# Optimization experiments

Hardware: AMD Instinct MI355X
Metric: run time of the kernel (lower is better)

Reference implementation:

```python
import jax, jax.numpy as jnp
import numpy as np

N_EMBD = 512
HEAD_SIZE = 64
T = 4096
B = 4


def setup_inputs() -> dict:
    key = jax.random.key(0)
    kx, kq, kk, kv = jax.random.split(key, 4)
    x = jax.random.normal(kx, (B, T, N_EMBD), dtype=jnp.float32)
    # torch nn.Linear(n_embd, head_size, bias=False): weight [head_size, n_embd];
    # stored here transposed as [n_embd, head_size] so projection is x @ W.
    s = 1.0 / np.sqrt(N_EMBD)
    Wq = jax.random.uniform(kq, (N_EMBD, HEAD_SIZE), jnp.float32, -s, s)
    Wk = jax.random.uniform(kk, (N_EMBD, HEAD_SIZE), jnp.float32, -s, s)
    Wv = jax.random.uniform(kv, (N_EMBD, HEAD_SIZE), jnp.float32, -s, s)
    return {"x": x, "Wq": Wq, "Wk": Wk, "Wv": Wv}


def reference(x, Wq, Wk, Wv):
    Bq, Tq, C = x.shape
    q = x @ Wq  # [B,T,H]
    k = x @ Wk  # [B,T,H]
    v = x @ Wv  # [B,T,H]
    # NOTE: original scales by C**-0.5 with C = n_embd (input dim), not head_size.
    wei = jnp.einsum('bqh,bkh->bqk', q, k) * (C ** -0.5)  # [B,T,T]
    causal = jnp.tril(jnp.ones((Tq, Tq), dtype=bool))
    wei = jnp.where(causal, wei, -jnp.inf)
    wei = jax.nn.softmax(wei, axis=-1)
    # dropout p=0.0 -> identity (eval-mode deterministic baseline)
    out = jnp.einsum('bqk,bkh->bqh', wei, v)  # [B,T,H]
    return out
```

## Files before the change

kernel.cpp:

```cpp
#include <hip/hip_runtime.h>
#include <hip/hip_bf16.h>
#include <math.h>

#define T_SEQ 4096
#define NBATCH 4
#define C_EMB 512
#define HEAD 64
#define CHUNK 8
#define EPB 288

typedef __attribute__((ext_vector_type(8))) short short8;
typedef __attribute__((ext_vector_type(4))) short short4v;
typedef __attribute__((ext_vector_type(4))) float f32x4;

#define C2 (0.044194173824159216f * 1.44269504088896340736f)

__device__ __forceinline__ unsigned short f2bf(float f) {
    union { float f; unsigned u; } v; v.f = f;
    unsigned u = v.u;
    u += 0x7FFF + ((u >> 16) & 1);
    return (unsigned short)(u >> 16);
}
__device__ __forceinline__ unsigned pk2bf(float a, float b) {
    __hip_bfloat162 h = __float22bfloat162_rn(make_float2(a, b));
    return *(unsigned*)&h;
}

__global__ __launch_bounds__(64) void wcvt_kernel(
    const float* __restrict__ Wq, const float* __restrict__ Wk,
    const float* __restrict__ Wv, unsigned short* __restrict__ wt)
{
    const int w = blockIdx.x >> 6;
    const int n = blockIdx.x & 63;
    const float* W = (w == 0) ? Wq : (w == 1) ? Wk : Wv;
    const int k0 = threadIdx.x * 8;
    unsigned short tmp[8];
#pragma unroll
    for (int i = 0; i < 8; ++i) tmp[i] = f2bf(W[(size_t)(k0 + i) * HEAD + n]);
    *(short8*)(wt + ((size_t)blockIdx.x) * C_EMB + k0) = *(short8*)tmp;
}

__device__ __forceinline__ void ld_stage(const float* xp, int s, float4* xr) {
#pragma unroll
    for (int j = 0; j < 4; ++j) {
        xr[2 * j]     = *(const float4*)(xp + (s * 4 + j) * 32);
        xr[2 * j + 1] = *(const float4*)(xp + (s * 4 + j) * 32 + 4);
    }
}

__device__ __forceinline__ void mm_stage(const float4* xr, int s, int l16, int quad,
                                         const unsigned short* __restrict__ wt,
                                         f32x4 acc[3][4]) {
#pragma unroll
    for (int j = 0; j < 4; ++j) {
        const int kc = s * 4 + j;
        float4 a = xr[2 * j], b = xr[2 * j + 1];
        int4 ai = make_int4((int)pk2bf(a.x, a.y), (int)pk2bf(a.z, a.w),
                            (int)pk2bf(b.x, b.y), (int)pk2bf(b.z, b.w));
        short8 af = *(short8*)&ai;
#pragma unroll
        for (int w = 0; w < 3; ++w)
#pragma unroll
            for (int n = 0; n < 4; ++n) {
                short8 bf = *(const short8*)(wt + ((size_t)(w * 64 + n * 16 + l16)) * C_EMB
                                                + kc * 32 + quad * 8);
                acc[w][n] = __builtin_amdgcn_mfma_f32_16x16x32_bf16(af, bf, acc[w][n], 0, 0, 0);
            }
    }
}

__global__ __launch_bounds__(256) void proj_kernel(
    const float* __restrict__ x,
    const unsigned short* __restrict__ wt,
    unsigned short* __restrict__ qout,
    unsigned short* __restrict__ kout,
    unsigned short* __restrict__ vt)
{
    __shared__ unsigned short Vsh[64][72];

    const int tid  = threadIdx.x;
    const int wave = tid >> 6;
    const int lane = tid & 63;
    const int l16  = lane & 15;
    const int quad = lane >> 4;
    const int row0 = blockIdx.x * 64;
    const int rowW = row0 + wave * 16 + l16;

    f32x4 acc[3][4];
#pragma unroll
    for (int w = 0; w < 3; ++w)
#pragma unroll
        for (int n = 0; n < 4; ++n) acc[w][n] = (f32x4){0.f, 0.f, 0.f, 0.f};

    const float* xp = x + (size_t)rowW * C_EMB + quad * 8;
    float4 xr[2][8];
    ld_stage(xp, 0, xr[0]);
#pragma unroll
    for (int s = 0; s < 4; ++s) {
        if (s < 3) ld_stage(xp, s + 1, xr[(s + 1) & 1]);
        mm_stage(xr[s & 1], s, l16, quad, wt, acc);
    }

#pragma unroll
    for (int n = 0; n < 4; ++n)
#pragma unroll
        for (int r = 0; r < 4; ++r) {
            int row = row0 + wave * 16 + quad * 4 + r;
            qout[(size_t)row * HEAD + n * 16 + l16] = f2bf(acc[0][n][r] * C2);
            kout[(size_t)row * HEAD + n * 16 + l16] = f2bf(acc[1][n][r]);
        }

#pragma unroll
    for (int n = 0; n < 4; ++n)
#pragma unroll
        for (int r = 0; r < 4; ++r)
            Vsh[n * 16 + l16][wave * 16 + quad * 4 + r] = f2bf(acc[2][n][r]);
    __syncthreads();
    {
        int h  = tid >> 2;
        int tc = (tid & 3) * 16;
        int b  = row0 >> 12;
        int t0 = row0 & (T_SEQ - 1);
        unsigned short* dst = vt + ((size_t)(b * HEAD + h)) * T_SEQ + t0 + tc;
        *(short8*)dst       = *(const short8*)&Vsh[h][tc];
        *(short8*)(dst + 8) = *(const short8*)&Vsh[h][tc + 8];
    }
}

__device__ __forceinline__ void stage_v(unsigned short (*Vbuf)[72], int sr, int phiA,
                                        short8 v0, short8 v1) {
    *(short4v*)&Vbuf[sr][phiA]      = __builtin_shufflevector(v0, v0, 0, 1, 2, 3);
    *(short4v*)&Vbuf[sr][phiA + 8]  = __builtin_shufflevector(v0, v0, 4, 5, 6, 7);
    *(short4v*)&Vbuf[sr][phiA + 16] = __builtin_shufflevector(v1, v1, 0, 1, 2, 3);
    *(short4v*)&Vbuf[sr][phiA + 24] = __builtin_shufflevector(v1, v1, 4, 5, 6, 7);
}

__global__ __launch_bounds__(256) void attn1_kernel(
    const unsigned short* __restrict__ qb,
    const unsigned short* __restrict__ kb,
    const unsigned short* __restrict__ vt,
    float* __restrict__ po,
    float* __restrict__ pl)
{
    __shared__ unsigned short Ks[2][64][72];
    __shared__ unsigned short Vs[2][64][72];

    const int tid  = threadIdx.x;
    const int wave = tid >> 6;
    const int lane = tid & 63;
    const int l16  = lane & 15;
    const int quad = lane >> 4;

    const int b = blockIdx.x / EPB;
    const int e = blockIdx.x % EPB;
    int g = 0;
#pragma unroll
    for (int gg = 1; gg < 8; ++gg) if (e >= 4 * gg * (gg + 1)) g = gg;
    const int rem = e - 4 * g * (g + 1);
    const int t   = rem / (g + 1);
    const int c   = rem - t * (g + 1);
    const int qt  = 8 * g + t;

    const size_t base = (size_t)b * T_SEQ;
    const int qrow = qt * 64 + wave * 16 + l16;
    short8 aq0 = *(const short8*)(qb + (base + qrow) * HEAD + quad * 8);
    short8 aq1 = *(const short8*)(qb + (base + qrow) * HEAD + 32 + quad * 8);

    float lacc = 0.f;
    f32x4 o[4];
#pragma unroll
    for (int n = 0; n < 4; ++n) o[n] = (f32x4){0.f, 0.f, 0.f, 0.f};

    const int kt0 = c * CHUNK;
    const int np  = min(CHUNK, qt + 1 - kt0);

    const int sr   = tid >> 2;
    const int sc   = (tid & 3) * 16;
    const int phiA = (sc & 32) + ((sc & 16) >> 2);

    short8 kra, krb, vra, vrb;
    {
        const int kbase = kt0 * 64;
        const unsigned short* ksrc = kb + (base + kbase + sr) * HEAD + sc;
        const unsigned short* vsrc = vt + ((size_t)(b * HEAD + sr)) * T_SEQ + kbase + sc;
        kra = *(const short8*)(ksrc);     krb = *(const short8*)(ksrc + 8);
        vra = *(const short8*)(vsrc);     vrb = *(const short8*)(vsrc + 8);
    }
    *(short8*)&Ks[0][sr][sc]     = kra;  *(short8*)&Ks[0][sr][sc + 8] = krb;
    stage_v(Vs[0], sr, phiA, vra, vrb);

    for (int p = 0; p < np; ++p) {
        const int cur = p & 1;
        const int kbase = (kt0 + p) * 64;
        __syncthreads();

        if (p + 1 < np) {
            const int nb = kbase + 64;
            const unsigned short* ksrc = kb + (base + nb + sr) * HEAD + sc;
            const unsigned short* vsrc = vt + ((size_t)(b * HEAD + sr)) * T_SEQ + nb + sc;
            kra = *(const short8*)(ksrc);  krb = *(const short8*)(ksrc + 8);
            vra = *(const short8*)(vsrc);  vrb = *(const short8*)(vsrc + 8);
        }

        f32x4 s[4];
#pragma unroll
        for (int n = 0; n < 4; ++n) {
            short8 bk0 = *(const short8*)&Ks[cur][n * 16 + l16][quad * 8];
            short8 bk1 = *(const short8*)&Ks[cur][n * 16 + l16][32 + quad * 8];
            f32x4 accS = (f32x4){0.f, 0.f, 0.f, 0.f};
            accS = __builtin_amdgcn_mfma_f32_16x16x32_bf16(bk0, aq0, accS, 0, 0, 0);
            accS = __builtin_amdgcn_mfma_f32_16x16x32_bf16(bk1, aq1, accS, 0, 0, 0);
            s[n] = accS;
        }

#pragma unroll
        for (int n = 0; n < 4; ++n)
#pragma unroll
            for (int r = 0; r < 4; ++r)
                s[n][r] = __builtin_amdgcn_exp2f(s[n][r]);

        if (kbase + 64 > qt * 64) {
            const int cb = kbase + quad * 4;
#pragma unroll
            for (int n = 0; n < 4; ++n)
#pragma unroll
                for (int r = 0; r < 4; ++r)
                    if (cb + n * 16 + r > qrow) s[n][r] = 0.f;
        }

#pragma unroll
        for (int n = 0; n < 4; ++n)
            lacc += (s[n][0] + s[n][1]) + (s[n][2] + s[n][3]);

#pragma unroll
        for (int st = 0; st < 2; ++st) {
            int4 ai = make_int4(
                (int)pk2bf(s[2 * st][0],     s[2 * st][1]),
                (int)pk2bf(s[2 * st][2],     s[2 * st][3]),
                (int)pk2bf(s[2 * st + 1][0], s[2 * st + 1][1]),
                (int)pk2bf(s[2 * st + 1][2], s[2 * st + 1][3]));
            short8 af = *(short8*)&ai;
#pragma unroll
            for (int n = 0; n < 4; ++n) {
                short8 bv = *(const short8*)&Vs[cur][n * 16 + l16][32 * st + quad * 8];
                o[n] = __builtin_amdgcn_mfma_f32_16x16x32_bf16(af, bv, o[n], 0, 0, 0);
            }
        }

        if (p + 1 < np) {
            const int nxt = cur ^ 1;
            *(short8*)&Ks[nxt][sr][sc]     = kra;  *(short8*)&Ks[nxt][sr][sc + 8] = krb;
            stage_v(Vs[nxt], sr, phiA, vra, vrb);
        }
    }

    lacc += __shfl_xor(lacc, 16);
    lacc += __shfl_xor(lacc, 32);

    const int pid = blockIdx.x;
#pragma unroll
    for (int n = 0; n < 4; ++n)
#pragma unroll
        for (int r = 0; r < 4; ++r) {
            int lr = wave * 16 + quad * 4 + r;
            po[(size_t)pid * 4096 + lr * 64 + n * 16 + l16] = o[n][r];
        }
    if (quad == 0)
        pl[pid * 64 + wave * 16 + l16] = lacc;
}

__global__ __launch_bounds__(256) void combine_kernel(
    const float* __restrict__ po, const float* __restrict__ pl,
    float* __restrict__ out)
{
    const int gth = blockIdx.x * 256 + threadIdx.x;
    const int h4  = gth & 15;
    const int row = gth >> 4;
    const int lr  = row & 63;
    const int qt  = (row >> 6) & 63;
    const int b   = row >> 12;
    const int nc  = (qt >> 3) + 1;
    const int g   = qt >> 3;
    const int rem = qt & 7;
    const int e0  = 4 * g * (g + 1) + rem * (g + 1);
    const int pid0 = b * EPB + e0;

    float l = 0.f;
    float4 acc = make_float4(0.f, 0.f, 0.f, 0.f);
    for (int cc = 0; cc < nc; ++cc) {
        l += pl[(pid0 + cc) * 64 + lr];
        float4 p4 = *(const float4*)(po + (size_t)(pid0 + cc) * 4096 + lr * 64 + h4 * 4);
        acc.x += p4.x; acc.y += p4.y; acc.z += p4.z; acc.w += p4.w;
    }
    float inv = 1.f / l;
    float4 res = make_float4(acc.x * inv, acc.y * inv, acc.z * inv, acc.w * inv);
    *(float4*)(out + (size_t)gth * 4) = res;
}

extern "C" void kernel_launch(void* const* d_in, const int* in_sizes, int n_in,
                              void* d_out, int out_size, void* d_ws, size_t ws_size,
                              hipStream_t stream) {
    const float* x  = (const float*)d_in[0];
    const float* Wq = (const float*)d_in[1];
    const float* Wk = (const float*)d_in[2];
    const float* Wv = (const float*)d_in[3];
    float* out = (float*)d_out;

    char* ws = (char*)d_ws;
    unsigned short* qb = (unsigned short*)(ws);
    unsigned short* kb = (unsigned short*)(ws + (2u << 20));
    unsigned short* vt = (unsigned short*)(ws + (4u << 20));
    unsigned short* wt = (unsigned short*)(ws + (6u << 20));
    float* pl = (float*)(ws + (6u << 20) + 196608);
    float* po = (float*)(ws + (6u << 20) + 196608 + 294912);

    wcvt_kernel<<<dim3(192), dim3(64), 0, stream>>>(Wq, Wk, Wv, wt);
    proj_kernel<<<dim3(256), dim3(256), 0, stream>>>(x, wt, qb, kb, vt);
    attn1_kernel<<<dim3(NBATCH * EPB), dim3(256), 0, stream>>>(qb, kb, vt, po, pl);
    combine_kernel<<<dim3(1024), dim3(256), 0, stream>>>(po, pl, out);
}
```

Measured before the change: 128.4 us.

## Split projection across waves by output column and store attention partials in bf16

The projection kernel now handles 32 rows per block, not 64. Its four waves split both the rows and the 192 output columns, so each wave holds 6 accumulators instead of 12. This doubles the grid to 512 blocks and sets a 2-blocks-per-SM launch bound, aiming for better occupancy. Separately, the split-KV attention partial outputs are written as bf16 instead of fp32 and the combine kernel reads them 8 at a time, halving the partial-output traffic at some cost in accuracy.

```diff
diff --git a/kernel.cpp b/kernel.cpp
--- a/kernel.cpp
+++ b/kernel.cpp
@@ -24,6 +24,10 @@
 __device__ __forceinline__ unsigned pk2bf(float a, float b) {
     __hip_bfloat162 h = __float22bfloat162_rn(make_float2(a, b));
     return *(unsigned*)&h;
+}
+__device__ __forceinline__ float bf2f(unsigned short u) {
+    union { unsigned u; float f; } v; v.u = ((unsigned)u) << 16;
+    return v.f;
 }
 
 __global__ __launch_bounds__(64) void wcvt_kernel(
@@ -49,8 +53,9 @@
 }
 
 __device__ __forceinline__ void mm_stage(const float4* xr, int s, int l16, int quad,
+                                         int gbase,
                                          const unsigned short* __restrict__ wt,
-                                         f32x4 acc[3][4]) {
+                                         f32x4 acc[6]) {
 #pragma unroll
     for (int j = 0; j < 4; ++j) {
         const int kc = s * 4 + j;
@@ -59,38 +64,37 @@
                             (int)pk2bf(b.x, b.y), (int)pk2bf(b.z, b.w));
         short8 af = *(short8*)&ai;
 #pragma unroll
-        for (int w = 0; w < 3; ++w)
-#pragma unroll
-            for (int n = 0; n < 4; ++n) {
-                short8 bf = *(const short8*)(wt + ((size_t)(w * 64 + n * 16 + l16)) * C_EMB
-                                                + kc * 32 + quad * 8);
-                acc[w][n] = __builtin_amdgcn_mfma_f32_16x16x32_bf16(af, bf, acc[w][n], 0, 0, 0);
-            }
-    }
-}
-
-__global__ __launch_bounds__(256) void proj_kernel(
+        for (int t = 0; t < 6; ++t) {
+            short8 bf = *(const short8*)(wt + ((size_t)((gbase + t) * 16 + l16)) * C_EMB
+                                            + kc * 32 + quad * 8);
+            acc[t] = __builtin_amdgcn_mfma_f32_16x16x32_bf16(af, bf, acc[t], 0, 0, 0);
+        }
+    }
+}
+
+__global__ __launch_bounds__(256, 2) void proj_kernel(
     const float* __restrict__ x,
     const unsigned short* __restrict__ wt,
     unsigned short* __restrict__ qout,
     unsigned short* __restrict__ kout,
     unsigned short* __restrict__ vt)
 {
-    __shared__ unsigned short Vsh[64][72];
-
-    const int tid  = threadIdx.x;
-    const int wave = tid >> 6;
-    const int lane = tid & 63;
-    const int l16  = lane & 15;
-    const int quad = lane >> 4;
-    const int row0 = blockIdx.x * 64;
-    const int rowW = row0 + wave * 16 + l16;
-
-    f32x4 acc[3][4];
-#pragma unroll
-    for (int w = 0; w < 3; ++w)
-#pragma unroll
-        for (int n = 0; n < 4; ++n) acc[w][n] = (f32x4){0.f, 0.f, 0.f, 0.f};
+    __shared__ unsigned short Vsh[64][40];
+
+    const int tid    = threadIdx.x;
+    const int wave   = tid >> 6;
+    const int lane   = tid & 63;
+    const int l16    = lane & 15;
+    const int quad   = lane >> 4;
+    const int rowblk = wave & 1;
+    const int wgroup = wave >> 1;
+    const int gbase  = wgroup * 6;
+    const int row0   = blockIdx.x * 32;
+    const int rowW   = row0 + rowblk * 16 + l16;
+
+    f32x4 acc[6];
+#pragma unroll
+    for (int t = 0; t < 6; ++t) acc[t] = (f32x4){0.f, 0.f, 0.f, 0.f};
 
     const float* xp = x + (size_t)rowW * C_EMB + quad * 8;
     float4 xr[2][8];
@@ -98,32 +102,34 @@
 #pragma unroll
     for (int s = 0; s < 4; ++s) {
         if (s < 3) ld_stage(xp, s + 1, xr[(s + 1) & 1]);
-        mm_stage(xr[s & 1], s, l16, quad, wt, acc);
-    }
-
-#pragma unroll
-    for (int n = 0; n < 4; ++n)
-#pragma unroll
-        for (int r = 0; r < 4; ++r) {
-            int row = row0 + wave * 16 + quad * 4 + r;
-            qout[(size_t)row * HEAD + n * 16 + l16] = f2bf(acc[0][n][r] * C2);
-            kout[(size_t)row * HEAD + n * 16 + l16] = f2bf(acc[1][n][r]);
-        }
-
-#pragma unroll
-    for (int n = 0; n < 4; ++n)
-#pragma unroll
-        for (int r = 0; r < 4; ++r)
-            Vsh[n * 16 + l16][wave * 16 + quad * 4 + r] = f2bf(acc[2][n][r]);
+        mm_stage(xr[s & 1], s, l16, quad, gbase, wt, acc);
+    }
+
+#pragma unroll
+    for (int r = 0; r < 4; ++r) {
+        const int row = row0 + rowblk * 16 + quad * 4 + r;
+        if (wgroup == 0) {
+#pragma unroll
+            for (int j = 0; j < 4; ++j)
+                qout[(size_t)row * HEAD + j * 16 + l16] = f2bf(acc[j][r] * C2);
+            kout[(size_t)row * HEAD + 0 * 16 + l16] = f2bf(acc[4][r]);
+            kout[(size_t)row * HEAD + 1 * 16 + l16] = f2bf(acc[5][r]);
+        } else {
+            kout[(size_t)row * HEAD + 2 * 16 + l16] = f2bf(acc[0][r]);
+            kout[(size_t)row * HEAD + 3 * 16 + l16] = f2bf(acc[1][r]);
+#pragma unroll
+            for (int j = 2; j < 6; ++j)
+                Vsh[(j - 2) * 16 + l16][rowblk * 16 + quad * 4 + r] = f2bf(acc[j][r]);
+        }
+    }
     __syncthreads();
     {
         int h  = tid >> 2;
-        int tc = (tid & 3) * 16;
+        int tc = (tid & 3) * 8;
         int b  = row0 >> 12;
         int t0 = row0 & (T_SEQ - 1);
         unsigned short* dst = vt + ((size_t)(b * HEAD + h)) * T_SEQ + t0 + tc;
-        *(short8*)dst       = *(const short8*)&Vsh[h][tc];
-        *(short8*)(dst + 8) = *(const short8*)&Vsh[h][tc + 8];
+        *(short8*)dst = *(const short8*)&Vsh[h][tc];
     }
 }
 
@@ -139,7 +145,7 @@
     const unsigned short* __restrict__ qb,
     const unsigned short* __restrict__ kb,
     const unsigned short* __restrict__ vt,
-    float* __restrict__ po,
+    unsigned short* __restrict__ po,
     float* __restrict__ pl)
 {
     __shared__ unsigned short Ks[2][64][72];
@@ -263,19 +269,19 @@
 #pragma unroll
         for (int r = 0; r < 4; ++r) {
             int lr = wave * 16 + quad * 4 + r;
-            po[(size_t)pid * 4096 + lr * 64 + n * 16 + l16] = o[n][r];
+            po[(size_t)pid * 4096 + lr * 64 + n * 16 + l16] = f2bf(o[n][r]);
         }
     if (quad == 0)
         pl[pid * 64 + wave * 16 + l16] = lacc;
 }
 
 __global__ __launch_bounds__(256) void combine_kernel(
-    const float* __restrict__ po, const float* __restrict__ pl,
+    const unsigned short* __restrict__ po, const float* __restrict__ pl,
     float* __restrict__ out)
 {
     const int gth = blockIdx.x * 256 + threadIdx.x;
-    const int h4  = gth & 15;
-    const int row = gth >> 4;
+    const int h8  = gth & 7;
+    const int row = gth >> 3;
     const int lr  = row & 63;
     const int qt  = (row >> 6) & 63;
     const int b   = row >> 12;
@@ -286,15 +292,21 @@
     const int pid0 = b * EPB + e0;
 
     float l = 0.f;
-    float4 acc = make_float4(0.f, 0.f, 0.f, 0.f);
+    float acc[8];
+#pragma unroll
+    for (int i = 0; i < 8; ++i) acc[i] = 0.f;
     for (int cc = 0; cc < nc; ++cc) {
         l += pl[(pid0 + cc) * 64 + lr];
-        float4 p4 = *(const float4*)(po + (size_t)(pid0 + cc) * 4096 + lr * 64 + h4 * 4);
-        acc.x += p4.x; acc.y += p4.y; acc.z += p4.z; acc.w += p4.w;
+        short8 p8 = *(const short8*)(po + (size_t)(pid0 + cc) * 4096 + lr * 64 + h8 * 8);
+#pragma unroll
+        for (int i = 0; i < 8; ++i) acc[i] += bf2f((unsigned short)p8[i]);
     }
     float inv = 1.f / l;
-    float4 res = make_float4(acc.x * inv, acc.y * inv, acc.z * inv, acc.w * inv);
-    *(float4*)(out + (size_t)gth * 4) = res;
+    float4 r0 = make_float4(acc[0] * inv, acc[1] * inv, acc[2] * inv, acc[3] * inv);
+    float4 r1 = make_float4(acc[4] * inv, acc[5] * inv, acc[6] * inv, acc[7] * inv);
+    float* dst = out + (size_t)gth * 8;
+    *(float4*)dst       = r0;
+    *(float4*)(dst + 4) = r1;
 }
 
 extern "C" void kernel_launch(void* const* d_in, const int* in_sizes, int n_in,
@@ -312,10 +324,10 @@
     unsigned short* vt = (unsigned short*)(ws + (4u << 20));
     unsigned short* wt = (unsigned short*)(ws + (6u << 20));
     float* pl = (float*)(ws + (6u << 20) + 196608);
-    float* po = (float*)(ws + (6u << 20) + 196608 + 294912);
+    unsigned short* po = (unsigned short*)(ws + (6u << 20) + 196608 + 294912);
 
     wcvt_kernel<<<dim3(192), dim3(64), 0, stream>>>(Wq, Wk, Wv, wt);
-    proj_kernel<<<dim3(256), dim3(256), 0, stream>>>(x, wt, qb, kb, vt);
+    proj_kernel<<<dim3(512), dim3(256), 0, stream>>>(x, wt, qb, kb, vt);
     attn1_kernel<<<dim3(NBATCH * EPB), dim3(256), 0, stream>>>(qb, kb, vt, po, pl);
-    combine_kernel<<<dim3(1024), dim3(256), 0, stream>>>(po, pl, out);
-}
+    combine_kernel<<<dim3(512), dim3(256), 0, stream>>>(po, pl, out);
+}
```

Result: slower. 136.0 us (+5.9%).
